# Optimization experiments

Hardware: AMD Instinct MI355X
Metric: run time of the kernel (lower is better)

The kernel has to match this reference:

```python
import jax, jax.numpy as jnp
import numpy as np


def setup_inputs() -> dict:
    key = jax.random.key(0)
    k1, k2 = jax.random.split(key)
    qs = jax.random.normal(k1, (8, 4096, 1024), dtype=jnp.float32)      # [B, L, D]
    memory = jax.random.normal(k2, (512, 1024), dtype=jnp.float32)       # [M, D]
    return {"qs": qs, "memory": memory}


def reference(qs, memory):
    # s = qs @ memory.T  -> [B, L, M]; permute -> [B, M, L]
    s = jnp.einsum("bld,md->bml", qs, memory)
    # softmax over L (last dim after permute)
    v = jax.nn.softmax(s, axis=2)                 # [B, M, L]
    # r = v @ qs -> [B, M, D]
    r = jnp.einsum("bml,bld->bmd", v, qs)
    return (r, memory)
```

## Files before the change

### kernel.cpp

```cpp
#include <hip/hip_runtime.h>
#include <hip/hip_fp16.h>


#define B_ 8
#define L_ 4096
#define D_ 1024
#define M_ 512

typedef _Float16 halfT;
typedef _Float16 half8 __attribute__((ext_vector_type(8)));
typedef _Float16 half4_t __attribute__((ext_vector_type(4)));
typedef float f32x4 __attribute__((ext_vector_type(4)));

#define OFF_MEM16 0ull
#define SZ_MEM16  (512ull*1024*2)
#define OFF_QS16  (OFF_MEM16 + SZ_MEM16)
#define SZ_QS16   (8ull*4096*1024*2)
#define OFF_S     (OFF_QS16 + SZ_QS16)
#define SZ_S      (8ull*512*4096*4)
#define OFF_P16   (OFF_S + SZ_S)
#define SZ_P16    (8ull*512*4096*2)
#define OFF_INVL  (OFF_P16 + SZ_P16)
#define SZ_INVL   (8ull*512*4)
#define WS_NEED   (OFF_INVL + SZ_INVL)
#define OFF_RP    OFF_S

#define SWZ(n) ((((n)&7) ^ (((n)>>5)&7)))

__device__ __forceinline__ void gload_lds16(const halfT* g, halfT* l) {
  __builtin_amdgcn_global_load_lds(
      (const __attribute__((address_space(1))) unsigned int*)(const void*)g,
      (__attribute__((address_space(3))) unsigned int*)l, 16, 0, 0);
}

__global__ void prep_mem16(const float* __restrict__ mem, halfT* __restrict__ mem16) {
  int i = blockIdx.x*256 + threadIdx.x;
  mem16[i] = (halfT)mem[i];
}

__global__ __launch_bounds__(256)
void prep_qs16(const float* __restrict__ qs, halfT* __restrict__ q16) {
  size_t base = (size_t)blockIdx.x*256 + threadIdx.x;
  #pragma unroll
  for (int it = 0; it < 8; ++it) {
    size_t e = (base + (size_t)it*524288)*8;
    f32x4 x0 = *(const f32x4*)&qs[e];
    f32x4 x1 = *(const f32x4*)&qs[e + 4];
    half8 h;
    #pragma unroll
    for (int j = 0; j < 4; ++j) { h[j] = (halfT)x0[j]; h[4+j] = (halfT)x1[j]; }
    *(half8*)&q16[e] = h;
  }
}

__global__ __launch_bounds__(512, 2)
void gemm_qk(const halfT* __restrict__ mem16, const halfT* __restrict__ qs16,
             float* __restrict__ S)
{
  __shared__ __attribute__((aligned(16))) halfT At[2][256*64];
  __shared__ __attribute__((aligned(16))) halfT Bt[2][256*64];

  int bid = blockIdx.x;
  int swz = (bid & 7)*32 + (bid >> 3);
  int b   = swz >> 5;
  int rem = swz & 31;
  int nt  = rem >> 1;
  int mt  = rem & 1;

  int tid = threadIdx.x;
  int w = tid >> 6, lane = tid & 63, lg = lane >> 4, li = lane & 15;
  int wm = w >> 2, wn = w & 3;
  int rA = tid >> 3;
  int cA = (tid & 7)*8;

  const halfT* Ab = mem16 + (size_t)mt*256*1024;
  const halfT* Bb = qs16 + ((size_t)b*L_ + nt*256)*D_;

  f32x4 acc[8][4];
  #pragma unroll
  for (int i=0;i<8;++i)
    #pragma unroll
    for (int j=0;j<4;++j) acc[i][j] = (f32x4){0.f,0.f,0.f,0.f};

#define STAGE_QK(nb_, kt_)                                                     \
  do {                                                                         \
    const halfT* a0 = Ab + (size_t)(kt_)*64 + cA;                              \
    const halfT* b0 = Bb + (size_t)(kt_)*64 + cA;                              \
    _Pragma("unroll")                                                          \
    for (int j = 0; j < 4; ++j) {                                              \
      int r = rA + j*64;                                                       \
      gload_lds16(a0 + (size_t)r*1024, &At[nb_][(tid + j*512)*8]);             \
      gload_lds16(b0 + (size_t)r*1024, &Bt[nb_][(tid + j*512)*8]);             \
    }                                                                          \
  } while (0)

  STAGE_QK(0, 0);
  __syncthreads();

  int nb = 0;
  for (int kt = 0; kt < 16; ++kt) {
    if (kt + 1 < 16) STAGE_QK(nb ^ 1, kt + 1);
    #pragma unroll
    for (int ksub = 0; ksub < 2; ++ksub) {
      half8 Af[8], Bf[4];
      #pragma unroll
      for (int mf = 0; mf < 8; ++mf)
        Af[mf] = *(const half8*)&At[nb][(wm*128 + mf*16 + li)*64 + ksub*32 + lg*8];
      #pragma unroll
      for (int nf = 0; nf < 4; ++nf)
        Bf[nf] = *(const half8*)&Bt[nb][(wn*64 + nf*16 + li)*64 + ksub*32 + lg*8];
      #pragma unroll
      for (int mf = 0; mf < 8; ++mf)
        #pragma unroll
        for (int nf = 0; nf < 4; ++nf)
          acc[mf][nf] = __builtin_amdgcn_mfma_f32_16x16x32_f16(Af[mf], Bf[nf], acc[mf][nf], 0,0,0);
    }
    __syncthreads();
    nb ^= 1;
  }
#undef STAGE_QK

  float* Cb = S + (size_t)b*M_*L_;
  int colbase = nt*256 + wn*64;
  #pragma unroll
  for (int mf = 0; mf < 8; ++mf) {
    #pragma unroll
    for (int r = 0; r < 4; ++r) {
      int row = mt*256 + wm*128 + mf*16 + lg*4 + r;
      #pragma unroll
      for (int nf = 0; nf < 4; ++nf)
        Cb[(size_t)row*L_ + colbase + nf*16 + li] = acc[mf][nf][r];
    }
  }
}

__global__ __launch_bounds__(512, 2)
void gemm_pv(const halfT* __restrict__ P16, const halfT* __restrict__ qs16,
             float* __restrict__ rp)
{
  __shared__ __attribute__((aligned(16))) halfT At[2][256*64];
  __shared__ __attribute__((aligned(16))) halfT Bt[2][256*64];

  int bid = blockIdx.x;
  int swz = (bid & 7)*32 + (bid >> 3);
  int ks  = swz >> 6;
  int rem = swz & 63;
  int b   = rem >> 3;
  int nt  = (rem >> 1) & 3;
  int mt  = rem & 1;

  int tid = threadIdx.x;
  int w = tid >> 6, lane = tid & 63, lg = lane >> 4, li = lane & 15;
  int wm = w >> 2, wn = w & 3;

  const halfT* Ab = P16 + (size_t)b*M_*L_ + (size_t)mt*256*L_ + ks*1024;
  const halfT* Bb = qs16 + ((size_t)b*L_ + ks*1024)*D_ + nt*256;
  int krow = tid >> 3;
  int seg  = tid & 7;

  f32x4 acc[8][4];
  #pragma unroll
  for (int i=0;i<8;++i)
    #pragma unroll
    for (int j=0;j<4;++j) acc[i][j] = (f32x4){0.f,0.f,0.f,0.f};

  half8 hx[4];

#define GLOADB_PV(kt_)                                                         \
  do {                                                                         \
    const halfT* src = Bb + (size_t)((kt_)*64 + krow)*D_ + seg*32;             \
    _Pragma("unroll")                                                          \
    for (int j = 0; j < 4; ++j) hx[j] = *(const half8*)(src + j*8);            \
  } while (0)

#define STAGEA_PV(nb_, kt_)                                                    \
  do {                                                                         \
    const halfT* a0 = Ab + (size_t)(kt_)*64 + (tid & 7)*8;                     \
    _Pragma("unroll")                                                          \
    for (int j = 0; j < 4; ++j)                                                \
      gload_lds16(a0 + (size_t)((tid >> 3) + j*64)*L_, &At[nb_][(tid + j*512)*8]); \
  } while (0)

#define WRITEB_PV(nb_)                                                         \
  do {                                                                         \
    _Pragma("unroll")                                                          \
    for (int i = 0; i < 32; ++i) {                                             \
      int n_ = seg*32 + i;                                                     \
      Bt[nb_][n_*64 + ((((krow >> 3) ^ SWZ(n_)) << 3)) + (krow & 7)] =         \
          hx[i >> 3][i & 7];                                                   \
    }                                                                          \
  } while (0)

  GLOADB_PV(0);
  STAGEA_PV(0, 0);
  WRITEB_PV(0);
  __syncthreads();

  int nb = 0;
  for (int kt = 0; kt < 16; ++kt) {
    if (kt + 1 < 16) { GLOADB_PV(kt + 1); STAGEA_PV(nb ^ 1, kt + 1); }
    #pragma unroll
    for (int ksub = 0; ksub < 2; ++ksub) {
      half8 Af[8], Bf[4];
      #pragma unroll
      for (int mf = 0; mf < 8; ++mf)
        Af[mf] = *(const half8*)&At[nb][(wm*128 + mf*16 + li)*64 + ksub*32 + lg*8];
      #pragma unroll
      for (int nf = 0; nf < 4; ++nf) {
        int n_ = wn*64 + nf*16 + li;
        Bf[nf] = *(const half8*)&Bt[nb][n_*64 + (((ksub*4 + lg) ^ SWZ(n_)) << 3)];
      }
      #pragma unroll
      for (int mf = 0; mf < 8; ++mf)
        #pragma unroll
        for (int nf = 0; nf < 4; ++nf)
          acc[mf][nf] = __builtin_amdgcn_mfma_f32_16x16x32_f16(Af[mf], Bf[nf], acc[mf][nf], 0,0,0);
    }
    if (kt + 1 < 16) WRITEB_PV(nb ^ 1);
    __syncthreads();
    nb ^= 1;
  }
#undef GLOADB_PV
#undef STAGEA_PV
#undef WRITEB_PV

  float* Cb = rp + (size_t)ks*((size_t)B_*M_*D_) + (size_t)b*M_*D_;
  int colbase = nt*256 + wn*64;
  #pragma unroll
  for (int mf = 0; mf < 8; ++mf) {
    #pragma unroll
    for (int r = 0; r < 4; ++r) {
      int row = mt*256 + wm*128 + mf*16 + lg*4 + r;
      #pragma unroll
      for (int nf = 0; nf < 4; ++nf)
        Cb[(size_t)row*D_ + colbase + nf*16 + li] = acc[mf][nf][r];
    }
  }
}

__global__ __launch_bounds__(256)
void softmax_rows(const float* __restrict__ S, halfT* __restrict__ P,
                  float* __restrict__ invl)
{
  __shared__ float red[4];
  int row = blockIdx.x;
  int tid = threadIdx.x;
  const float* src = S + (size_t)row*L_;
  f32x4 v[4];
  float mx = -3.0e38f;
  #pragma unroll
  for (int i = 0; i < 4; ++i) {
    v[i] = *(const f32x4*)&src[(size_t)(i*256 + tid)*4];
    #pragma unroll
    for (int e = 0; e < 4; ++e) mx = fmaxf(mx, v[i][e]);
  }
  #pragma unroll
  for (int off = 1; off < 64; off <<= 1) mx = fmaxf(mx, __shfl_xor(mx, off));
  int w = tid >> 6;
  if ((tid & 63) == 0) red[w] = mx;
  __syncthreads();
  mx = fmaxf(fmaxf(red[0], red[1]), fmaxf(red[2], red[3]));

  float sum = 0.f;
  halfT* dst = P + (size_t)row*L_;
  #pragma unroll
  for (int i = 0; i < 4; ++i) {
    half4_t h;
    #pragma unroll
    for (int e = 0; e < 4; ++e) {
      float ev = __expf(v[i][e] - mx);
      sum += ev;
      h[e] = (halfT)ev;
    }
    *(half4_t*)&dst[(size_t)(i*256 + tid)*4] = h;
  }
  #pragma unroll
  for (int off = 1; off < 64; off <<= 1) sum += __shfl_xor(sum, off);
  __syncthreads();
  if ((tid & 63) == 0) red[w] = sum;
  __syncthreads();
  if (tid == 0) invl[row] = 1.0f / (red[0] + red[1] + red[2] + red[3]);
}

__global__ __launch_bounds__(256)
void combine_scale(const float* __restrict__ rp, const float* __restrict__ invl,
                   float* __restrict__ out)
{
  int bm = blockIdx.x;
  int tid = threadIdx.x;
  size_t off = (size_t)bm*D_ + tid*4;
  f32x4 v = *(const f32x4*)&rp[off];
  #pragma unroll
  for (int s = 1; s < 4; ++s)
    v += *(const f32x4*)&rp[(size_t)s*B_*M_*D_ + off];
  float sc = invl[bm];
  v *= sc;
  *(f32x4*)&out[off] = v;
}

__global__ void fallback_kernel(const float* __restrict__ qs,
                                const float* __restrict__ mem,
                                float* __restrict__ out)
{
  __shared__ float w_lds[4][4096];
  __shared__ float mem_s[4][1024];
  __shared__ float redb[256];
  int blk = blockIdx.x;
  int b = blk >> 7;
  int m0 = (blk & 127)*4;
  int tid = threadIdx.x;

  for (int i = tid; i < 4*1024; i += 256)
    mem_s[i>>10][i&1023] = mem[(size_t)(m0 + (i>>10))*D_ + (i&1023)];
  __syncthreads();

  float mx[4] = {-3e38f,-3e38f,-3e38f,-3e38f};
  for (int l = tid; l < L_; l += 256) {
    const float* qp = qs + ((size_t)b*L_ + l)*D_;
    float dot[4] = {0,0,0,0};
    for (int dd = 0; dd < D_; dd += 4) {
      f32x4 qv = *(const f32x4*)(qp + dd);
      #pragma unroll
      for (int mi=0; mi<4; ++mi)
        dot[mi] += qv[0]*mem_s[mi][dd] + qv[1]*mem_s[mi][dd+1]
                 + qv[2]*mem_s[mi][dd+2] + qv[3]*mem_s[mi][dd+3];
    }
    #pragma unroll
    for (int mi=0; mi<4; ++mi) { w_lds[mi][l] = dot[mi]; mx[mi] = fmaxf(mx[mi], dot[mi]); }
  }
  float Mv[4], Zv[4];
  for (int mi=0; mi<4; ++mi) {
    redb[tid] = mx[mi]; __syncthreads();
    for (int s=128; s>0; s>>=1) { if (tid<s) redb[tid]=fmaxf(redb[tid],redb[tid+s]); __syncthreads(); }
    Mv[mi] = redb[0]; __syncthreads();
  }
  float sm[4] = {0,0,0,0};
  for (int l = tid; l < L_; l += 256)
    #pragma unroll
    for (int mi=0; mi<4; ++mi) {
      float wv = __expf(w_lds[mi][l] - Mv[mi]);
      w_lds[mi][l] = wv; sm[mi] += wv;
    }
  for (int mi=0; mi<4; ++mi) {
    redb[tid] = sm[mi]; __syncthreads();
    for (int s=128; s>0; s>>=1) { if (tid<s) redb[tid]+=redb[tid+s]; __syncthreads(); }
    Zv[mi] = redb[0]; __syncthreads();
  }
  int d0 = tid*4;
  f32x4 a[4];
  #pragma unroll
  for (int mi=0;mi<4;++mi) a[mi] = (f32x4){0,0,0,0};
  for (int l = 0; l < L_; ++l) {
    f32x4 qv = *(const f32x4*)(qs + ((size_t)b*L_ + l)*D_ + d0);
    #pragma unroll
    for (int mi=0; mi<4; ++mi) a[mi] += qv * w_lds[mi][l];
  }
  #pragma unroll
  for (int mi=0; mi<4; ++mi) {
    float invz = 1.f/Zv[mi];
    #pragma unroll
    for (int c=0; c<4; ++c)
      out[((size_t)b*M_ + m0 + mi)*D_ + d0 + c] = a[mi][c]*invz;
  }
}

extern "C" void kernel_launch(void* const* d_in, const int* in_sizes, int n_in,
                              void* d_out, int out_size, void* d_ws, size_t ws_size,
                              hipStream_t stream) {
  const float* qs  = (const float*)d_in[0];
  const float* mem = (const float*)d_in[1];
  float* out = (float*)d_out;

  hipMemcpyAsync(out + (size_t)B_*M_*D_, mem, (size_t)M_*D_*sizeof(float),
                 hipMemcpyDeviceToDevice, stream);

  if (ws_size >= (size_t)WS_NEED) {
    char* base = (char*)d_ws;
    halfT* mem16 = (halfT*)(base + OFF_MEM16);
    halfT* qs16  = (halfT*)(base + OFF_QS16);
    float* S     = (float*)(base + OFF_S);
    halfT* P16   = (halfT*)(base + OFF_P16);
    float* invl  = (float*)(base + OFF_INVL);
    float* rp    = (float*)(base + OFF_RP);

    prep_mem16<<<2048, 256, 0, stream>>>(mem, mem16);
    prep_qs16<<<2048, 256, 0, stream>>>(qs, qs16);
    gemm_qk<<<256, 512, 0, stream>>>(mem16, qs16, S);
    softmax_rows<<<4096, 256, 0, stream>>>(S, P16, invl);
    gemm_pv<<<256, 512, 0, stream>>>(P16, qs16, rp);
    combine_scale<<<4096, 256, 0, stream>>>(rp, invl, out);
  } else {
    fallback_kernel<<<1024, 256, 0, stream>>>(qs, mem, out);
  }
}
```

Measured before the change: 175.7 us.

## Pre-swizzle fp16 operands in global memory to remove LDS bank conflicts

The fp16 conversion kernels and the softmax now write their outputs with an XOR swizzle of 8-element groups within each 64-wide k-tile, keyed on row index. The direct global-to-LDS loads then land in LDS already swizzled, so the MFMA fragment reads in both GEMMs index with the matching XOR and avoid bank conflicts. The B-operand global load in gemm_pv is adjusted to un-swizzle the qs16 layout. prep_mem16 is also vectorized to 8 elements per thread with fewer blocks.

Measured after the change: 165.6 us. 5.7% less time.

```diff
diff --git a/kernel.cpp b/kernel.cpp
--- a/kernel.cpp
+++ b/kernel.cpp
@@ -33,9 +33,18 @@
       (__attribute__((address_space(3))) unsigned int*)l, 16, 0, 0);
 }
 
-__global__ void prep_mem16(const float* __restrict__ mem, halfT* __restrict__ mem16) {
-  int i = blockIdx.x*256 + threadIdx.x;
-  mem16[i] = (halfT)mem[i];
+__global__ __launch_bounds__(256)
+void prep_mem16(const float* __restrict__ mem, halfT* __restrict__ mem16) {
+  int i8 = blockIdx.x*256 + threadIdx.x;
+  int row = i8 >> 7, c = i8 & 127;
+  int kt = c >> 3, g = c & 7;
+  const float* src = mem + (size_t)i8*8;
+  f32x4 x0 = *(const f32x4*)src;
+  f32x4 x1 = *(const f32x4*)(src + 4);
+  half8 h;
+  #pragma unroll
+  for (int j = 0; j < 4; ++j) { h[j] = (halfT)x0[j]; h[4+j] = (halfT)x1[j]; }
+  *(half8*)&mem16[(size_t)row*1024 + kt*64 + ((g ^ (row & 7)) << 3)] = h;
 }
 
 __global__ __launch_bounds__(256)
@@ -43,13 +52,17 @@
   size_t base = (size_t)blockIdx.x*256 + threadIdx.x;
   #pragma unroll
   for (int it = 0; it < 8; ++it) {
-    size_t e = (base + (size_t)it*524288)*8;
-    f32x4 x0 = *(const f32x4*)&qs[e];
-    f32x4 x1 = *(const f32x4*)&qs[e + 4];
+    size_t i8 = base + (size_t)it*524288;
+    size_t row = i8 >> 7;
+    int c = (int)(i8 & 127);
+    int kt = c >> 3, g = c & 7;
+    const float* src = qs + i8*8;
+    f32x4 x0 = *(const f32x4*)src;
+    f32x4 x1 = *(const f32x4*)(src + 4);
     half8 h;
     #pragma unroll
     for (int j = 0; j < 4; ++j) { h[j] = (halfT)x0[j]; h[4+j] = (halfT)x1[j]; }
-    *(half8*)&q16[e] = h;
+    *(half8*)&q16[row*1024 + kt*64 + ((g ^ ((int)row & 7)) << 3)] = h;
   }
 }
 
@@ -70,6 +83,7 @@
   int tid = threadIdx.x;
   int w = tid >> 6, lane = tid & 63, lg = lane >> 4, li = lane & 15;
   int wm = w >> 2, wn = w & 3;
+  int sl = li & 7;
   int rA = tid >> 3;
   int cA = (tid & 7)*8;
 
@@ -102,13 +116,14 @@
     if (kt + 1 < 16) STAGE_QK(nb ^ 1, kt + 1);
     #pragma unroll
     for (int ksub = 0; ksub < 2; ++ksub) {
+      int gx = ((ksub*4 + lg) ^ sl) << 3;
       half8 Af[8], Bf[4];
       #pragma unroll
       for (int mf = 0; mf < 8; ++mf)
-        Af[mf] = *(const half8*)&At[nb][(wm*128 + mf*16 + li)*64 + ksub*32 + lg*8];
+        Af[mf] = *(const half8*)&At[nb][(wm*128 + mf*16 + li)*64 + gx];
       #pragma unroll
       for (int nf = 0; nf < 4; ++nf)
-        Bf[nf] = *(const half8*)&Bt[nb][(wn*64 + nf*16 + li)*64 + ksub*32 + lg*8];
+        Bf[nf] = *(const half8*)&Bt[nb][(wn*64 + nf*16 + li)*64 + gx];
       #pragma unroll
       for (int mf = 0; mf < 8; ++mf)
         #pragma unroll
@@ -152,11 +167,13 @@
   int tid = threadIdx.x;
   int w = tid >> 6, lane = tid & 63, lg = lane >> 4, li = lane & 15;
   int wm = w >> 2, wn = w & 3;
+  int sl = li & 7;
 
   const halfT* Ab = P16 + (size_t)b*M_*L_ + (size_t)mt*256*L_ + ks*1024;
   const halfT* Bb = qs16 + ((size_t)b*L_ + ks*1024)*D_ + nt*256;
   int krow = tid >> 3;
   int seg  = tid & 7;
+  int rs   = krow & 7;
 
   f32x4 acc[8][4];
   #pragma unroll
@@ -168,9 +185,10 @@
 
 #define GLOADB_PV(kt_)                                                         \
   do {                                                                         \
-    const halfT* src = Bb + (size_t)((kt_)*64 + krow)*D_ + seg*32;             \
+    const halfT* rowp = Bb + (size_t)((kt_)*64 + krow)*D_ + (seg >> 1)*64;     \
     _Pragma("unroll")                                                          \
-    for (int j = 0; j < 4; ++j) hx[j] = *(const half8*)(src + j*8);            \
+    for (int j = 0; j < 4; ++j)                                                \
+      hx[j] = *(const half8*)(rowp + ((((seg & 1)*4 + j) ^ rs) << 3));         \
   } while (0)
 
 #define STAGEA_PV(nb_, kt_)                                                    \
@@ -201,10 +219,11 @@
     if (kt + 1 < 16) { GLOADB_PV(kt + 1); STAGEA_PV(nb ^ 1, kt + 1); }
     #pragma unroll
     for (int ksub = 0; ksub < 2; ++ksub) {
+      int gx = ((ksub*4 + lg) ^ sl) << 3;
       half8 Af[8], Bf[4];
       #pragma unroll
       for (int mf = 0; mf < 8; ++mf)
-        Af[mf] = *(const half8*)&At[nb][(wm*128 + mf*16 + li)*64 + ksub*32 + lg*8];
+        Af[mf] = *(const half8*)&At[nb][(wm*128 + mf*16 + li)*64 + gx];
       #pragma unroll
       for (int nf = 0; nf < 4; ++nf) {
         int n_ = wn*64 + nf*16 + li;
@@ -244,6 +263,7 @@
 {
   __shared__ float red[4];
   int row = blockIdx.x;
+  int rs  = row & 7;
   int tid = threadIdx.x;
   const float* src = S + (size_t)row*L_;
   f32x4 v[4];
@@ -272,7 +292,9 @@
       sum += ev;
       h[e] = (halfT)ev;
     }
-    *(half4_t*)&dst[(size_t)(i*256 + tid)*4] = h;
+    int idx4 = i*256 + tid;
+    int kt = idx4 >> 4, g = (idx4 >> 1) & 7, o = idx4 & 1;
+    *(half4_t*)&dst[kt*64 + ((g ^ rs) << 3) + o*4] = h;
   }
   #pragma unroll
   for (int off = 1; off < 64; off <<= 1) sum += __shfl_xor(sum, off);
@@ -383,7 +405,7 @@
     float* invl  = (float*)(base + OFF_INVL);
     float* rp    = (float*)(base + OFF_RP);
 
-    prep_mem16<<<2048, 256, 0, stream>>>(mem, mem16);
+    prep_mem16<<<256, 256, 0, stream>>>(mem, mem16);
     prep_qs16<<<2048, 256, 0, stream>>>(qs, qs16);
     gemm_qk<<<256, 512, 0, stream>>>(mem16, qs16, S);
     softmax_rows<<<4096, 256, 0, stream>>>(S, P16, invl);
```
